# Optimization experiments

Hardware: AMD Instinct MI355X
Metric: run time of the kernel (lower is better)

Reference implementation:

```python
import jax, jax.numpy as jnp
import numpy as np

HEADS = 12
D_HEAD = 64  # d_model // heads


def _split_heads(t, heads, d_head):
    # Faithful to the torch code: transpose(1,2) -> (B, C, T), then
    # reshape (B, -1, heads, d_head), then transpose(1,2) -> (B, heads, T', d_head).
    B = t.shape[0]
    t = jnp.swapaxes(t, 1, 2)                      # (B, C, T)
    t = t.reshape(B, -1, heads, d_head)            # (B, T', heads, d_head) -- layout quirk preserved
    return jnp.swapaxes(t, 1, 2)                   # (B, heads, T', d_head)


def setup_inputs() -> dict:
    key = jax.random.key(0)
    ks = jax.random.split(key, 10)
    B, Tq, Tkv, D = 8, 4096, 77, 768
    s = 0.02
    return {
        "x": jax.random.normal(ks[0], (B, Tq, D), jnp.float32),
        "prompt": jax.random.normal(ks[1], (B, Tkv, D), jnp.float32),
        "Wq": jax.random.normal(ks[2], (D, D), jnp.float32) * s,
        "bq": jax.random.normal(ks[3], (D,), jnp.float32) * s,
        "Wk": jax.random.normal(ks[4], (D, D), jnp.float32) * s,
        "bk": jax.random.normal(ks[5], (D,), jnp.float32) * s,
        "Wv": jax.random.normal(ks[6], (D, D), jnp.float32) * s,
        "bv": jax.random.normal(ks[7], (D,), jnp.float32) * s,
        "Wp": jax.random.normal(ks[8], (D, D), jnp.float32) * s,
        "bp": jax.random.normal(ks[9], (D,), jnp.float32) * s,
    }


def reference(x, prompt, Wq, bq, Wk, bk, Wv, bv, Wp, bp):
    B, Tq, C = x.shape
    Ckv = prompt.shape[-1]
    q = _split_heads(x @ Wq.T + bq, HEADS, D_HEAD)       # (B, H, Tq, d_head)
    k = _split_heads(prompt @ Wk.T + bk, HEADS, D_HEAD)  # (B, H, Tkv, d_head)
    v = _split_heads(prompt @ Wv.T + bv, HEADS, D_HEAD)
    scale = 1.0 / jnp.sqrt(jnp.asarray(Ckv, x.dtype))    # note: sqrt(d_prompt), as in source
    att = jnp.einsum('bhqd,bhkd->bhqk', q, k) * scale
    att = jax.nn.softmax(att, axis=-1)
    out = jnp.einsum('bhqk,bhkd->bhqd', att, v)          # (B, H, Tq, d_head)
    out = jnp.swapaxes(out, 1, 2).reshape(B, Tq, C)
    return out @ Wp.T + bp                               # dropout = identity (eval)
```

## Files before the change

kernel.cpp:

```cpp
#include <hip/hip_runtime.h>

typedef __attribute__((ext_vector_type(8))) __bf16 bf16x8;
typedef __attribute__((ext_vector_type(4))) float f32x4;
typedef __attribute__((ext_vector_type(8))) unsigned short u16x8;
typedef __attribute__((ext_vector_type(4))) unsigned short u16x4;

#define DEV __device__ __forceinline__

DEV float bf2f(unsigned short u) {
  unsigned int x = ((unsigned int)u) << 16;
  return __builtin_bit_cast(float, x);
}
DEV unsigned short f2bf(float f) {
  unsigned int u = __builtin_bit_cast(unsigned int, f);
  u = u + 0x7fffu + ((u >> 16) & 1u);
  return (unsigned short)(u >> 16);
}

DEV void glds16(const void* g, void* l) {
  __builtin_amdgcn_global_load_lds(
      (__attribute__((address_space(1))) void*)g,
      (__attribute__((address_space(3))) void*)l, 16, 0, 0);
}

__global__ __launch_bounds__(256) void k_prep(
    const float* __restrict__ x, const float* __restrict__ Wq,
    const float* __restrict__ Wk, const float* __restrict__ Wv,
    const float* __restrict__ Wp, const float* __restrict__ prompt,
    const float* __restrict__ bk, const float* __restrict__ bv,
    unsigned short* __restrict__ xb, unsigned short* __restrict__ wqb,
    unsigned short* __restrict__ wkvb, unsigned short* __restrict__ wpb,
    unsigned short* __restrict__ pb, float* __restrict__ bkv) {
  const int blk = blockIdx.x;
  const int tid = threadIdx.x;
  if (blk < 2048) {
    for (int i = blk * 256 + tid; i < 6291456; i += 524288) {
      float4 v = reinterpret_cast<const float4*>(x)[i];
      u16x4 o;
      o[0] = f2bf(v.x); o[1] = f2bf(v.y); o[2] = f2bf(v.z); o[3] = f2bf(v.w);
      reinterpret_cast<u16x4*>(xb)[i] = o;
    }
  } else if (blk < 4352) {
    const int w = (blk - 2048) / 576;
    const int i = (blk - 2048 - w * 576) * 256 + tid;
    const float* src = (w == 0) ? Wq : (w == 1) ? Wk : (w == 2) ? Wv : Wp;
    unsigned short* dst =
        (w == 0) ? wqb : (w == 1) ? wkvb : (w == 2) ? (wkvb + 589824) : wpb;
    float4 v = reinterpret_cast<const float4*>(src)[i];
    u16x4 o;
    o[0] = f2bf(v.x); o[1] = f2bf(v.y); o[2] = f2bf(v.z); o[3] = f2bf(v.w);
    reinterpret_cast<u16x4*>(dst)[i] = o;
  } else if (blk < 5120) {
    const int i4 = (blk - 4352) * 256 + tid;
    const int e = i4 * 4;
    const int b = e / 98304;
    const int rem = e - b * 98304;
    const int s = rem / 768;
    const int d = rem - s * 768;
    u16x4 o;
    if (s < 77) {
      float4 v = *reinterpret_cast<const float4*>(&prompt[((long)b * 77 + s) * 768 + d]);
      o[0] = f2bf(v.x); o[1] = f2bf(v.y); o[2] = f2bf(v.z); o[3] = f2bf(v.w);
    } else {
      o[0] = 0; o[1] = 0; o[2] = 0; o[3] = 0;
    }
    reinterpret_cast<u16x4*>(pb)[i4] = o;
  } else {
    const int i = (blk - 5120) * 256 + tid;
    bkv[i] = (i < 768) ? bk[i] : bv[i - 768];
  }
}

__global__ __launch_bounds__(256, 2) void k_gemmkv(const unsigned short* __restrict__ A,
                                                   const unsigned short* __restrict__ B, long sB,
                                                   unsigned short* __restrict__ Cv, long sC,
                                                   const float* __restrict__ bias) {
  __shared__ alignas(16) unsigned short As[128 * 64];
  __shared__ alignas(16) unsigned short Bs[128 * 64];

  const int bz = blockIdx.z;
  const unsigned short* Bb = B + (long)bz * sB;

  const int tid = threadIdx.x;
  const int wave = tid >> 6;
  const int lane = tid & 63;
  const int tm = blockIdx.y * 128;
  const int wm = (wave >> 1) * 64;
  const int wn = (wave & 1) * 64;
  const int fr = lane & 15;
  const int fk = (lane >> 4) * 8;
  const int srow = lane >> 3;
  const int scol = (lane & 7) * 8;

  f32x4 acc[4][4] = {};

  for (int k0 = 0; k0 < 768; k0 += 64) {
    __syncthreads();
#pragma unroll
    for (int i = 0; i < 4; ++i) {
      const int chunk = i * 4 + wave;
      glds16(A + (long)(tm + chunk * 8 + srow) * 768 + (k0 + scol), &As[chunk * 512]);
    }
#pragma unroll
    for (int i = 0; i < 4; ++i) {
      const int chunk = i * 4 + wave;
      glds16(Bb + (long)(chunk * 8 + srow) * 768 + (k0 + scol), &Bs[chunk * 512]);
    }
    __syncthreads();
#pragma unroll
    for (int ks = 0; ks < 2; ++ks) {
      bf16x8 af[4], bf[4];
#pragma unroll
      for (int mi = 0; mi < 4; ++mi)
        af[mi] = *reinterpret_cast<const bf16x8*>(&As[(wm + mi * 16 + fr) * 64 + ks * 32 + fk]);
#pragma unroll
      for (int ni = 0; ni < 4; ++ni)
        bf[ni] = *reinterpret_cast<const bf16x8*>(&Bs[(wn + ni * 16 + fr) * 64 + ks * 32 + fk]);
#pragma unroll
      for (int mi = 0; mi < 4; ++mi)
#pragma unroll
        for (int ni = 0; ni < 4; ++ni)
          acc[mi][ni] =
              __builtin_amdgcn_mfma_f32_16x16x32_bf16(af[mi], bf[ni], acc[mi][ni], 0, 0, 0);
    }
  }

  const int r0 = (lane >> 4) * 4;
#pragma unroll
  for (int mi = 0; mi < 4; ++mi) {
#pragma unroll
    for (int ni = 0; ni < 4; ++ni) {
      const int col = wn + ni * 16 + fr;
      if (col < 77) {
#pragma unroll
        for (int r = 0; r < 4; ++r) {
          const int row = tm + wm + mi * 16 + r0 + r;
          Cv[(long)bz * sC + (long)row * 77 + col] = f2bf(acc[mi][ni][r] + bias[row]);
        }
      }
    }
  }
}

template <int QUIRK>
__global__ __launch_bounds__(256, 2) void k_g128(const unsigned short* __restrict__ A,
                                                 const unsigned short* __restrict__ B,
                                                 void* __restrict__ Cv,
                                                 const float* __restrict__ bias) {
  __shared__ alignas(16) unsigned short S[17408];
  unsigned short* const As = S;
  unsigned short* const Bs = S + 8192;

  const int tid = threadIdx.x;
  const int wave = tid >> 6;
  const int lane = tid & 63;
  const int l = (blockIdx.x & 7) * 192 + (blockIdx.x >> 3);
  const int tm = (QUIRK ? (l % 6) : (l / 6)) * 128;
  const int tn = (QUIRK ? (l / 6) : (l % 6)) * 128;
  const int wm = (wave >> 1) * 64;
  const int wn = (wave & 1) * 64;
  const int fr = lane & 15;
  const int fk = (lane >> 4) * 8;
  const int srow = lane >> 3;
  const int srcx = ((lane & 7) ^ srow) * 8;
  const int rx = (fr & 7) * 8;

  f32x4 acc[4][4] = {};

  for (int k0 = 0; k0 < 768; k0 += 64) {
    __syncthreads();
#pragma unroll
    for (int i = 0; i < 4; ++i) {
      const int chunk = i * 4 + wave;
      glds16(A + (long)(tm + chunk * 8 + srow) * 768 + (k0 + srcx), &As[chunk * 512]);
    }
#pragma unroll
    for (int i = 0; i < 4; ++i) {
      const int chunk = i * 4 + wave;
      glds16(B + (long)(tn + chunk * 8 + srow) * 768 + (k0 + srcx), &Bs[chunk * 512]);
    }
    __syncthreads();
#pragma unroll
    for (int ks = 0; ks < 2; ++ks) {
      bf16x8 af[4], bf[4];
#pragma unroll
      for (int mi = 0; mi < 4; ++mi)
        af[mi] = *reinterpret_cast<const bf16x8*>(
            &As[(wm + mi * 16 + fr) * 64 + ((ks * 32 + fk) ^ rx)]);
#pragma unroll
      for (int ni = 0; ni < 4; ++ni)
        bf[ni] = *reinterpret_cast<const bf16x8*>(
            &Bs[(wn + ni * 16 + fr) * 64 + ((ks * 32 + fk) ^ rx)]);
#pragma unroll
      for (int mi = 0; mi < 4; ++mi)
#pragma unroll
        for (int ni = 0; ni < 4; ++ni)
          acc[mi][ni] =
              __builtin_amdgcn_mfma_f32_16x16x32_bf16(af[mi], bf[ni], acc[mi][ni], 0, 0, 0);
    }
  }

  const int r0 = (lane >> 4) * 4;

  if (QUIRK) {
    __syncthreads();
#pragma unroll
    for (int mi = 0; mi < 4; ++mi)
#pragma unroll
      for (int ni = 0; ni < 4; ++ni)
#pragma unroll
        for (int r = 0; r < 4; ++r) {
          const int cm = wm + mi * 16 + r0 + r;
          const int ct = wn + ni * 16 + fr;
          S[cm * 136 + ct] = f2bf(acc[mi][ni][r] + bias[tm + cm]);
        }
    __syncthreads();
    unsigned short* qt = (unsigned short*)Cv;
    const int b_ = tn >> 12;
    const int toff = tn & 4095;
    const int cm = tid >> 1;
    const int t8 = (tid & 1) * 64;
    const long gb = (long)b_ * 3145728 + (long)(tm + cm) * 4096 + toff + t8;
#pragma unroll
    for (int j = 0; j < 8; ++j)
      *reinterpret_cast<u16x8*>(&qt[gb + j * 8]) =
          *reinterpret_cast<const u16x8*>(&S[cm * 136 + t8 + j * 8]);
  } else {
    float* out = (float*)Cv;
#pragma unroll
    for (int mi = 0; mi < 4; ++mi) {
#pragma unroll
      for (int ni = 0; ni < 4; ++ni) {
        const int col = tn + wn + ni * 16 + fr;
        const float bv = bias[col];
#pragma unroll
        for (int r = 0; r < 4; ++r) {
          const long g = tm + wm + mi * 16 + r0 + r;
          out[g * 768 + col] = acc[mi][ni][r] + bv;
        }
      }
    }
  }
}

__global__ __launch_bounds__(256, 3) void k_attn(const unsigned short* __restrict__ QT,
                                                 const unsigned short* __restrict__ KVT,
                                                 unsigned short* __restrict__ Y) {
  __shared__ alignas(16) unsigned short Plds[128 * 104];
  __shared__ alignas(16) unsigned short Vt[64 * 104];

  const int b = blockIdx.z;
  const int h = blockIdx.y;
  const int tid = threadIdx.x;
  const int wave = tid >> 6;
  const int lane = tid & 63;
  const int fr = lane & 15;
  const int fg = lane >> 4;

  const long kvb = (long)b * 118272;
  const long kflat = kvb + h * 64;
  const long vflat = kvb + 59136 + h * 64;

  for (int task = tid; task < 1024; task += 256) {
    const int s8 = task & 15;
    if (s8 < 12) {
      const int d = task >> 4;
      u16x8 v;
#pragma unroll
      for (int j = 0; j < 8; ++j) {
        const int s = s8 * 8 + j;
        v[j] = (s < 77) ? KVT[vflat + (long)s * 768 + d] : (unsigned short)0;
      }
      *reinterpret_cast<u16x8*>(&Vt[d * 104 + s8 * 8]) = v;
    }
  }
  {
    const int row = wave * 32 + (lane >> 1);
    u16x8 z = {};
    *reinterpret_cast<u16x8*>(&Plds[row * 104 + 80 + (lane & 1) * 8]) = z;
  }

  const int t0 = blockIdx.x * 128 + wave * 32;
  const long qb = (long)b * 3145728 + h * 64;

  bf16x8 qa[2][2];
#pragma unroll
  for (int m = 0; m < 2; ++m)
#pragma unroll
    for (int ks = 0; ks < 2; ++ks)
      qa[m][ks] = *reinterpret_cast<const bf16x8*>(
          &QT[qb + (long)(t0 + m * 16 + fr) * 768 + ks * 32 + fg * 8]);

  bf16x8 kb[5][2];
#pragma unroll
  for (int n = 0; n < 5; ++n)
#pragma unroll
    for (int ks = 0; ks < 2; ++ks)
      kb[n][ks] = *reinterpret_cast<const bf16x8*>(
          &KVT[kflat + (long)(n * 16 + fr) * 768 + ks * 32 + fg * 8]);

  f32x4 s_[2][5] = {};
#pragma unroll
  for (int ks = 0; ks < 2; ++ks)
#pragma unroll
    for (int m = 0; m < 2; ++m)
#pragma unroll
      for (int n = 0; n < 5; ++n)
        s_[m][n] = __builtin_amdgcn_mfma_f32_16x16x32_bf16(qa[m][ks], kb[n][ks], s_[m][n], 0, 0, 0);

  const float scale = 0.036084391824351615f;
  f32x4 rl[2];
#pragma unroll
  for (int m = 0; m < 2; ++m) {
#pragma unroll
    for (int n = 0; n < 5; ++n) {
      const int key = n * 16 + fr;
#pragma unroll
      for (int r = 0; r < 4; ++r)
        s_[m][n][r] = (key < 77) ? __expf(s_[m][n][r] * scale) : 0.f;
    }
    f32x4 t = s_[m][0] + s_[m][1] + s_[m][2] + s_[m][3] + s_[m][4];
#pragma unroll
    for (int w = 1; w < 16; w <<= 1) {
      f32x4 u;
#pragma unroll
      for (int r = 0; r < 4; ++r) u[r] = __shfl_xor(t[r], w);
      t += u;
    }
    rl[m][0] = 1.f / t[0]; rl[m][1] = 1.f / t[1];
    rl[m][2] = 1.f / t[2]; rl[m][3] = 1.f / t[3];
  }

#pragma unroll
  for (int m = 0; m < 2; ++m)
#pragma unroll
    for (int n = 0; n < 5; ++n)
#pragma unroll
      for (int r = 0; r < 4; ++r)
        Plds[(wave * 32 + m * 16 + fg * 4 + r) * 104 + n * 16 + fr] = f2bf(s_[m][n][r]);

  __syncthreads();

  f32x4 o[2][4] = {};
#pragma unroll
  for (int ks = 0; ks < 3; ++ks) {
    bf16x8 pa[2], vb[4];
#pragma unroll
    for (int m = 0; m < 2; ++m)
      pa[m] = *reinterpret_cast<const bf16x8*>(
          &Plds[(wave * 32 + m * 16 + fr) * 104 + ks * 32 + fg * 8]);
#pragma unroll
    for (int n = 0; n < 4; ++n)
      vb[n] = *reinterpret_cast<const bf16x8*>(&Vt[(n * 16 + fr) * 104 + ks * 32 + fg * 8]);
#pragma unroll
    for (int m = 0; m < 2; ++m)
#pragma unroll
      for (int n = 0; n < 4; ++n)
        o[m][n] = __builtin_amdgcn_mfma_f32_16x16x32_bf16(pa[m], vb[n], o[m][n], 0, 0, 0);
  }

#pragma unroll
  for (int m = 0; m < 2; ++m)
#pragma unroll
    for (int n = 0; n < 4; ++n)
#pragma unroll
      for (int r = 0; r < 4; ++r) {
        const int t = t0 + m * 16 + fg * 4 + r;
        const int d = n * 16 + fr;
        Y[qb + (long)t * 768 + d] = f2bf(o[m][n][r] * rl[m][r]);
      }
}

extern "C" void kernel_launch(void* const* d_in, const int* in_sizes, int n_in,
                              void* d_out, int out_size, void* d_ws, size_t ws_size,
                              hipStream_t stream) {
  const float* x      = (const float*)d_in[0];
  const float* prompt = (const float*)d_in[1];
  const float* Wq     = (const float*)d_in[2];
  const float* bq     = (const float*)d_in[3];
  const float* Wk     = (const float*)d_in[4];
  const float* bk     = (const float*)d_in[5];
  const float* Wv     = (const float*)d_in[6];
  const float* bv     = (const float*)d_in[7];
  const float* Wp     = (const float*)d_in[8];
  const float* bp     = (const float*)d_in[9];
  float* out = (float*)d_out;

  if (ws_size < 108853248u) return;
  char* ws = (char*)d_ws;
  unsigned short* xb   = (unsigned short*)(ws + 0);
  unsigned short* y    = xb;
  unsigned short* qt   = (unsigned short*)(ws + 50331648L);
  unsigned short* wqb  = (unsigned short*)(ws + 100663296L);
  unsigned short* wpb  = (unsigned short*)(ws + 101842944L);
  unsigned short* wkvb = (unsigned short*)(ws + 103022592L);
  unsigned short* pb   = (unsigned short*)(ws + 105381888L);
  unsigned short* kvt  = (unsigned short*)(ws + 106954752L);
  float*          bkv  = (float*)(ws + 108847104L);

  k_prep<<<5126, 256, 0, stream>>>(x, Wq, Wk, Wv, Wp, prompt, bk, bv,
                                   xb, wqb, wkvb, wpb, pb, bkv);

  k_gemmkv<<<dim3(1, 12, 8), 256, 0, stream>>>(wkvb, pb, 98304L, kvt, 118272L, bkv);

  k_g128<1><<<1536, 256, 0, stream>>>(wqb, xb, qt, bq);

  k_attn<<<dim3(32, 12, 8), 256, 0, stream>>>(qt, kvt, y);

  k_g128<0><<<1536, 256, 0, stream>>>(y, wpb, out, bp);
}
```

Before: 201.1 us.

## Emit pre-transposed padded V from KV GEMM and stream it into attention LDS

The KV projection GEMM now writes V directly in a per-head transposed, padded layout (d x 104) into a separate buffer, which the prep kernel zero-fills first. The attention kernel loads this tile with 16-byte global-to-LDS copies instead of gathering scalar elements with a strided transpose in every block. The attention launch bound is also raised to 4 blocks per SM. The cost is scattered 2-byte stores in the small KV GEMM, extra zero-fill work, and more register pressure from the higher occupancy target.

```diff
diff --git a/kernel.cpp b/kernel.cpp
--- a/kernel.cpp
+++ b/kernel.cpp
@@ -30,7 +30,8 @@
     const float* __restrict__ bk, const float* __restrict__ bv,
     unsigned short* __restrict__ xb, unsigned short* __restrict__ wqb,
     unsigned short* __restrict__ wkvb, unsigned short* __restrict__ wpb,
-    unsigned short* __restrict__ pb, float* __restrict__ bkv) {
+    unsigned short* __restrict__ pb, float* __restrict__ bkv,
+    unsigned short* __restrict__ vt2) {
   const int blk = blockIdx.x;
   const int tid = threadIdx.x;
   if (blk < 2048) {
@@ -65,15 +66,20 @@
       o[0] = 0; o[1] = 0; o[2] = 0; o[3] = 0;
     }
     reinterpret_cast<u16x4*>(pb)[i4] = o;
+  } else if (blk < 5126) {
+    const int i = (blk - 5120) * 256 + tid;
+    if (i < 1536) bkv[i] = (i < 768) ? bk[i] : bv[i - 768];
   } else {
-    const int i = (blk - 5120) * 256 + tid;
-    bkv[i] = (i < 768) ? bk[i] : bv[i - 768];
+    const int i = (blk - 5126) * 256 + tid;
+    u16x8 z = {};
+    reinterpret_cast<u16x8*>(vt2)[i] = z;
   }
 }
 
 __global__ __launch_bounds__(256, 2) void k_gemmkv(const unsigned short* __restrict__ A,
                                                    const unsigned short* __restrict__ B, long sB,
-                                                   unsigned short* __restrict__ Cv, long sC,
+                                                   unsigned short* __restrict__ Kv,
+                                                   unsigned short* __restrict__ Vt2,
                                                    const float* __restrict__ bias) {
   __shared__ alignas(16) unsigned short As[128 * 64];
   __shared__ alignas(16) unsigned short Bs[128 * 64];
@@ -135,7 +141,15 @@
 #pragma unroll
         for (int r = 0; r < 4; ++r) {
           const int row = tm + wm + mi * 16 + r0 + r;
-          Cv[(long)bz * sC + (long)row * 77 + col] = f2bf(acc[mi][ni][r] + bias[row]);
+          const unsigned short v = f2bf(acc[mi][ni][r] + bias[row]);
+          if (tm < 768) {
+            Kv[(long)bz * 59136 + (long)row * 77 + col] = v;
+          } else {
+            const int p = (row - 768) * 77 + col;
+            const int snew = p / 768;
+            const int c0 = p - snew * 768;
+            Vt2[(long)bz * 79872 + (long)c0 * 104 + snew] = v;
+          }
         }
       }
     }
@@ -243,8 +257,9 @@
   }
 }
 
-__global__ __launch_bounds__(256, 3) void k_attn(const unsigned short* __restrict__ QT,
+__global__ __launch_bounds__(256, 4) void k_attn(const unsigned short* __restrict__ QT,
                                                  const unsigned short* __restrict__ KVT,
+                                                 const unsigned short* __restrict__ VT2,
                                                  unsigned short* __restrict__ Y) {
   __shared__ alignas(16) unsigned short Plds[128 * 104];
   __shared__ alignas(16) unsigned short Vt[64 * 104];
@@ -257,23 +272,13 @@
   const int fr = lane & 15;
   const int fg = lane >> 4;
 
-  const long kvb = (long)b * 118272;
-  const long kflat = kvb + h * 64;
-  const long vflat = kvb + 59136 + h * 64;
-
-  for (int task = tid; task < 1024; task += 256) {
-    const int s8 = task & 15;
-    if (s8 < 12) {
-      const int d = task >> 4;
-      u16x8 v;
-#pragma unroll
-      for (int j = 0; j < 8; ++j) {
-        const int s = s8 * 8 + j;
-        v[j] = (s < 77) ? KVT[vflat + (long)s * 768 + d] : (unsigned short)0;
-      }
-      *reinterpret_cast<u16x8*>(&Vt[d * 104 + s8 * 8]) = v;
-    }
-  }
+  const unsigned short* vsrc = VT2 + (long)b * 79872 + h * 6656;
+#pragma unroll
+  for (int r = 0; r < 4; ++r) {
+    const int chunk = r * 256 + tid;
+    if (chunk < 832) glds16(vsrc + chunk * 8, &Vt[chunk * 8]);
+  }
+
   {
     const int row = wave * 32 + (lane >> 1);
     u16x8 z = {};
@@ -282,6 +287,7 @@
 
   const int t0 = blockIdx.x * 128 + wave * 32;
   const long qb = (long)b * 3145728 + h * 64;
+  const long kflat = (long)b * 59136 + h * 64;
 
   bf16x8 qa[2][2];
 #pragma unroll
@@ -386,7 +392,7 @@
   const float* bp     = (const float*)d_in[9];
   float* out = (float*)d_out;
 
-  if (ws_size < 108853248u) return;
+  if (ws_size < 109185024u) return;
   char* ws = (char*)d_ws;
   unsigned short* xb   = (unsigned short*)(ws + 0);
   unsigned short* y    = xb;
@@ -396,16 +402,17 @@
   unsigned short* wkvb = (unsigned short*)(ws + 103022592L);
   unsigned short* pb   = (unsigned short*)(ws + 105381888L);
   unsigned short* kvt  = (unsigned short*)(ws + 106954752L);
-  float*          bkv  = (float*)(ws + 108847104L);
-
-  k_prep<<<5126, 256, 0, stream>>>(x, Wq, Wk, Wv, Wp, prompt, bk, bv,
-                                   xb, wqb, wkvb, wpb, pb, bkv);
-
-  k_gemmkv<<<dim3(1, 12, 8), 256, 0, stream>>>(wkvb, pb, 98304L, kvt, 118272L, bkv);
+  unsigned short* vt2  = (unsigned short*)(ws + 107900928L);
+  float*          bkv  = (float*)(ws + 109178880L);
+
+  k_prep<<<5438, 256, 0, stream>>>(x, Wq, Wk, Wv, Wp, prompt, bk, bv,
+                                   xb, wqb, wkvb, wpb, pb, bkv, vt2);
+
+  k_gemmkv<<<dim3(1, 12, 8), 256, 0, stream>>>(wkvb, pb, 98304L, kvt, vt2, bkv);
 
   k_g128<1><<<1536, 256, 0, stream>>>(wqb, xb, qt, bq);
 
-  k_attn<<<dim3(32, 12, 8), 256, 0, stream>>>(qt, kvt, y);
+  k_attn<<<dim3(32, 12, 8), 256, 0, stream>>>(qt, kvt, vt2, y);
 
   k_g128<0><<<1536, 256, 0, stream>>>(y, wpb, out, bp);
 }
```

Measured after the change: 193.0 us. 1.04x faster.
